# Kernel tuning notes

Measured on AMD Instinct MI355X. Metric: run time of the kernel, lower is better.

## Reference

```python
import math
import jax, jax.numpy as jnp
import numpy as np

B, N, L, D, H = 1, 64, 512, 768, 12
DK = D // H


def setup_inputs() -> dict:
    rng = jax.random.key(0)
    ks = jax.random.split(rng, 8)
    s = 0.02  # weight init scale
    return {
        "query": jax.random.normal(ks[0], (B, N, L, D), jnp.float32),
        "key": jax.random.normal(ks[1], (B, N, L, D), jnp.float32),
        "value": jax.random.normal(ks[2], (B, N, L, D), jnp.float32),
        "Wq": jax.random.normal(ks[3], (D, D), jnp.float32) * s,
        "bq": jnp.zeros((D,), jnp.float32),
        "Wk": jax.random.normal(ks[4], (D, D), jnp.float32) * s,
        "bk": jnp.zeros((D,), jnp.float32),
        "Wv": jax.random.normal(ks[5], (D, D), jnp.float32) * s,
        "bv": jnp.zeros((D,), jnp.float32),
        "Wo": jax.random.normal(ks[6], (D, D), jnp.float32) * s,
        "bo": jnp.zeros((D,), jnp.float32),
    }


def reference(query, key, value, Wq, bq, Wk, bk, Wv, bv, Wo, bo):
    b, n, l, d = query.shape
    h, dk = H, DK
    # combined scaling: 1/sqrt(d_k) * 1/sqrt(N)
    scale = 1.0 / (math.sqrt(dk) * math.sqrt(n))
    # nn.Linear: y = x @ W.T + b  (W is [out, in])
    q = (jnp.einsum('bnld,ed->bnle', query, Wq) + bq).reshape(b, n, l, h, dk) * scale
    k = (jnp.einsum('bnld,ed->bnle', key, Wk) + bk).reshape(b, n, l, h, dk)
    v = (jnp.einsum('bnld,ed->bnle', value, Wv) + bv).reshape(b, n, l, h, dk)
    # tied attention: scores summed over the N (sequence-copy) axis BEFORE softmax
    att = jnp.einsum('bnihk,bnjhk->bhij', q, k)  # [B,H,L,L]
    att = jax.nn.softmax(att, axis=-1)  # dropout is identity in eval
    # single attention map broadcast across all N value tensors
    out = jnp.einsum('bhij,bnjhk->bnihk', att, v).reshape(b, n, l, d)
    return jnp.einsum('bnld,ed->bnle', out, Wo) + bo
```

## Files before the change

kernel.cpp:

```cpp
#include <hip/hip_runtime.h>


typedef __bf16 bf16x8 __attribute__((ext_vector_type(8)));
typedef float f32x4 __attribute__((ext_vector_type(4)));

__device__ __forceinline__ unsigned short f2bf(float f) {
  unsigned u = __float_as_uint(f);
  u += 0x7fffu + ((u >> 16) & 1u);
  return (unsigned short)(u >> 16);
}

__device__ __forceinline__ void gll16(const unsigned short* g, unsigned short* l) {
  __builtin_amdgcn_global_load_lds(
      (const __attribute__((address_space(1))) unsigned int*)g,
      (__attribute__((address_space(3))) unsigned int*)l, 16, 0, 0);
}

#define VMCNT_4 asm volatile("s_waitcnt vmcnt(4)" ::: "memory")
#define VMCNT_0 asm volatile("s_waitcnt vmcnt(0)" ::: "memory")
#define BAR __builtin_amdgcn_s_barrier()

enum { MODE_QCAT = 0, MODE_VT = 1, MODE_ATT = 2, MODE_OUTWS = 3, MODE_OUT_BIAS = 4 };

constexpr int BM = 128, BN = 128, BK = 32;

template <int MODE, bool SWZ, int KS>
__global__ __launch_bounds__(256, 2) void gemm_bt(
    const void* __restrict__ Av, const void* __restrict__ Bv,
    const float* __restrict__ bias, void* __restrict__ Cv,
    int K, int lda, int ldb, long long a_bs, long long b_bs,
    float alpha, int ntn,
    const float* __restrict__ bias2, float alpha2, long long c_bs) {
  constexpr int LP = 32;

  __shared__ unsigned short As0[BM * LP];
  __shared__ unsigned short Bs0[BN * LP];
  __shared__ unsigned short As1[BM * LP];
  __shared__ unsigned short Bs1[BN * LP];

  const int tid = threadIdx.x;
  const int wave = tid >> 6;
  const int lane = tid & 63;
  const int wm = wave >> 1, wn = wave & 1;

  int tm, tn, batch = 0, ks = 0;
  if constexpr (SWZ && MODE == MODE_ATT) {
    const int bid = blockIdx.x;
    const int xcd = bid & 7, j = bid >> 3;
    const int z = (j >> 4) * 8 + xcd;
    const int tile = j & 15;
    tn = tile & 3;
    tm = tile >> 2;
    ks = z % KS;
    batch = z / KS;
  } else if constexpr (SWZ && MODE == MODE_OUTWS) {
    const int bid = blockIdx.x;
    const int xcd = bid & 7, j = bid >> 3;
    const int g = (j >> 6) * 8 + xcd;
    const int idx = j & 63;
    batch = g >> 1;
    tm = idx >> 4;
    tn = (g & 1) * 16 + (idx & 15);
  } else {
    if constexpr (SWZ) {
      const int bid = blockIdx.x;
      const int xcd = bid & 7;
      const int k = bid >> 3;
      tn = k % ntn;
      tm = (k / ntn) * 8 + xcd;
    } else {
      tn = blockIdx.x;
      tm = blockIdx.y;
    }
    batch = blockIdx.z;
    if constexpr (KS > 1) { ks = batch % KS; batch /= KS; }
  }

  const long long m0 = (long long)tm * BM;
  const long long n0 = (long long)tn * BN;

  const unsigned short* Ab = (const unsigned short*)Av + (long long)batch * a_bs + (long long)ks * K;
  const unsigned short* Bb = (const unsigned short*)Bv + (long long)batch * b_bs + (long long)ks * K;

  f32x4 acc[4][4] = {};

  const int l15 = lane & 15;
  const int kq = (lane >> 4) * 8;
  const int r_in = lane >> 2;
  const int c8 = (lane & 3) * 8;

  auto stage = [&](unsigned short* Asb, unsigned short* Bsb, int k0) {
#pragma unroll
    for (int t = 0; t < 2; ++t) {
      const int rb = t * 64 + wave * 16;
      gll16(Ab + (m0 + rb + r_in) * (long long)lda + k0 + c8, &Asb[rb * LP]);
      gll16(Bb + (n0 + rb + r_in) * (long long)ldb + k0 + c8, &Bsb[rb * LP]);
    }
  };
  auto compute = [&](const unsigned short* Asb, const unsigned short* Bsb) {
    bf16x8 af[4], bfr[4];
#pragma unroll
    for (int t = 0; t < 4; ++t)
      af[t] = *(const bf16x8*)&Asb[(wm * 64 + t * 16 + l15) * LP + kq];
#pragma unroll
    for (int u = 0; u < 4; ++u)
      bfr[u] = *(const bf16x8*)&Bsb[(wn * 64 + u * 16 + l15) * LP + kq];
#pragma unroll
    for (int t = 0; t < 4; ++t)
#pragma unroll
      for (int u = 0; u < 4; ++u)
        acc[t][u] = __builtin_amdgcn_mfma_f32_16x16x32_bf16(af[t], bfr[u], acc[t][u], 0, 0, 0);
  };

  float bpre[4] = {};
  float aa = alpha;
  if constexpr (MODE == MODE_QCAT) {
    const float* bb = batch ? bias2 : bias;
    aa = batch ? alpha2 : alpha;
#pragma unroll
    for (int u = 0; u < 4; ++u) bpre[u] = bb[n0 + wn * 64 + u * 16 + l15];
  } else if constexpr (MODE == MODE_VT || MODE == MODE_OUT_BIAS) {
#pragma unroll
    for (int u = 0; u < 4; ++u) bpre[u] = bias[n0 + wn * 64 + u * 16 + l15];
  }

  stage(As0, Bs0, 0);
  VMCNT_0;
  BAR;

  const int NT = K >> 5;
  for (int t = 0; t < NT; t += 2) {
    stage(As1, Bs1, (t + 1) << 5);
    VMCNT_4;
    BAR;
    compute(As0, Bs0);
    BAR;
    if (t + 2 < NT) {
      stage(As0, Bs0, (t + 2) << 5);
      VMCNT_4;
    } else {
      VMCNT_0;
    }
    BAR;
    compute(As1, Bs1);
    BAR;
  }

#pragma unroll
  for (int t = 0; t < 4; ++t) {
#pragma unroll
    for (int u = 0; u < 4; ++u) {
      const long long col = n0 + wn * 64 + u * 16 + l15;
#pragma unroll
      for (int r = 0; r < 4; ++r) {
        const long long row = m0 + wm * 64 + t * 16 + (lane >> 4) * 4 + r;
        float v = acc[t][u][r];
        if constexpr (MODE == MODE_QCAT) {
          v = (v + bpre[u]) * aa;
          const long long h = col >> 6, kk = col & 63, n = row >> 9, i = row & 511;
          ((unsigned short*)Cv + batch * c_bs)[((h * 512 + i) << 12) + (n << 6) + kk] = f2bf(v);
        } else if constexpr (MODE == MODE_VT) {
          v = v + bpre[u];
          const long long h = col >> 6, kk = col & 63, n = row >> 9, j = row & 511;
          ((unsigned short*)Cv)[(((h << 12) + (n << 6) + kk) << 9) + j] = f2bf(v);
        } else if constexpr (MODE == MODE_ATT) {
          float* p = &((float*)Cv)[((long long)batch << 18) + (row << 9) + col];
          if constexpr (KS > 1) atomicAdd(p, v); else *p = v;
        } else if constexpr (MODE == MODE_OUTWS) {
          const long long n = col >> 6, kk = col & 63;
          ((unsigned short*)Cv)[(n * 512 + row) * 768 + (long long)batch * 64 + kk] = f2bf(v);
        } else {
          ((float*)Cv)[row * 768 + col] = v + bpre[u];
        }
      }
    }
  }
}

__global__ __launch_bounds__(256) void softmax_rows(const float* __restrict__ att,
                                                    unsigned short* __restrict__ outb) {
  const long long rowbase = (long long)blockIdx.x << 9;
  const int tid = threadIdx.x;
  float a = att[rowbase + tid];
  float b = att[rowbase + tid + 256];

  float m = fmaxf(a, b);
#pragma unroll
  for (int off = 32; off; off >>= 1) m = fmaxf(m, __shfl_down(m, off));
  __shared__ float redm[4];
  if ((tid & 63) == 0) redm[tid >> 6] = m;
  __syncthreads();
  m = fmaxf(fmaxf(redm[0], redm[1]), fmaxf(redm[2], redm[3]));

  const float e0 = __expf(a - m), e1 = __expf(b - m);
  float s = e0 + e1;
#pragma unroll
  for (int off = 32; off; off >>= 1) s += __shfl_down(s, off);
  __shared__ float reds[4];
  if ((tid & 63) == 0) reds[tid >> 6] = s;
  __syncthreads();
  s = reds[0] + reds[1] + reds[2] + reds[3];

  const float inv = 1.0f / s;
  outb[rowbase + tid] = f2bf(e0 * inv);
  outb[rowbase + tid + 256] = f2bf(e1 * inv);
}

__global__ __launch_bounds__(256) void cvt_bf16(const float* __restrict__ in,
                                                unsigned short* __restrict__ out) {
  const long long i = ((long long)blockIdx.x * 256 + threadIdx.x) * 8;
  const float4 a = *(const float4*)(in + i);
  const float4 b = *(const float4*)(in + i + 4);
  uint4 p;
  p.x = (unsigned)f2bf(a.x) | ((unsigned)f2bf(a.y) << 16);
  p.y = (unsigned)f2bf(a.z) | ((unsigned)f2bf(a.w) << 16);
  p.z = (unsigned)f2bf(b.x) | ((unsigned)f2bf(b.y) << 16);
  p.w = (unsigned)f2bf(b.z) | ((unsigned)f2bf(b.w) << 16);
  *(uint4*)(out + i) = p;
}

__global__ __launch_bounds__(256) void cvt_qk(
    const float* __restrict__ s0, const float* __restrict__ s1,
    unsigned short* __restrict__ d0, unsigned short* __restrict__ d1) {
  const float* s = blockIdx.y ? s1 : s0;
  unsigned short* d = blockIdx.y ? d1 : d0;
  const long long i = ((long long)blockIdx.x * 256 + threadIdx.x) * 8;
  const float4 a = *(const float4*)(s + i);
  const float4 b = *(const float4*)(s + i + 4);
  uint4 p;
  p.x = (unsigned)f2bf(a.x) | ((unsigned)f2bf(a.y) << 16);
  p.y = (unsigned)f2bf(a.z) | ((unsigned)f2bf(a.w) << 16);
  p.z = (unsigned)f2bf(b.x) | ((unsigned)f2bf(b.y) << 16);
  p.w = (unsigned)f2bf(b.z) | ((unsigned)f2bf(b.w) << 16);
  *(uint4*)(d + i) = p;
}

__global__ __launch_bounds__(256) void cvt_w4(
    const float* __restrict__ s0, const float* __restrict__ s1,
    const float* __restrict__ s2, const float* __restrict__ s3,
    unsigned short* __restrict__ d0, unsigned short* __restrict__ d1,
    unsigned short* __restrict__ d2, unsigned short* __restrict__ d3) {
  const float* s;
  unsigned short* d;
  switch (blockIdx.y) {
    case 0: s = s0; d = d0; break;
    case 1: s = s1; d = d1; break;
    case 2: s = s2; d = d2; break;
    default: s = s3; d = d3; break;
  }
  const long long i = ((long long)blockIdx.x * 256 + threadIdx.x) * 8;
  const float4 a = *(const float4*)(s + i);
  const float4 b = *(const float4*)(s + i + 4);
  uint4 p;
  p.x = (unsigned)f2bf(a.x) | ((unsigned)f2bf(a.y) << 16);
  p.y = (unsigned)f2bf(a.z) | ((unsigned)f2bf(a.w) << 16);
  p.z = (unsigned)f2bf(b.x) | ((unsigned)f2bf(b.y) << 16);
  p.w = (unsigned)f2bf(b.z) | ((unsigned)f2bf(b.w) << 16);
  *(uint4*)(d + i) = p;
}

extern "C" void kernel_launch(void* const* d_in, const int* in_sizes, int n_in,
                              void* d_out, int out_size, void* d_ws, size_t ws_size,
                              hipStream_t stream) {
  const float* query = (const float*)d_in[0];
  const float* key   = (const float*)d_in[1];
  const float* value = (const float*)d_in[2];
  const float* Wq = (const float*)d_in[3];
  const float* bq = (const float*)d_in[4];
  const float* Wk = (const float*)d_in[5];
  const float* bk = (const float*)d_in[6];
  const float* Wv = (const float*)d_in[7];
  const float* bv = (const float*)d_in[8];
  const float* Wo = (const float*)d_in[9];
  const float* bo = (const float*)d_in[10];
  float* out = (float*)d_out;

  char* ws = (char*)d_ws;
  unsigned short* q_ws  = (unsigned short*)(ws);
  unsigned short* k_ws  = (unsigned short*)(ws + 50331648);
  unsigned short* vt_ws = (unsigned short*)(ws + 100663296);
  float*          att   = (float*)(ws + 150994944);
  unsigned short* wo_b  = (unsigned short*)(ws + 163577856);
  unsigned short* wq_b  = (unsigned short*)(ws + 150994944);
  unsigned short* wk_b  = (unsigned short*)(ws + 150994944 + 1179648);
  unsigned short* wv_b  = (unsigned short*)(ws + 150994944 + 2359296);
  unsigned short* att_b = k_ws;
  unsigned short* out_ws = q_ws;
  unsigned short* xb0 = (unsigned short*)d_out;
  unsigned short* xb1 = (unsigned short*)d_out + 25165824;

  const dim3 blk(256);

  cvt_w4<<<dim3(288, 4), blk, 0, stream>>>(Wo, Wq, Wk, Wv, wo_b, wq_b, wk_b, wv_b);

  cvt_qk<<<dim3(12288, 2), blk, 0, stream>>>(query, key, xb0, xb1);

  gemm_bt<MODE_QCAT, true, 1><<<dim3(1536, 1, 2), blk, 0, stream>>>(
      xb0, wq_b, bq, q_ws, 768, 768, 768, 25165824LL, 589824LL, 0.015625f, 6,
      bk, 1.0f, 25165824LL);

  cvt_bf16<<<12288, blk, 0, stream>>>(value, xb0);
  gemm_bt<MODE_VT, true, 1><<<dim3(1536, 1, 1), blk, 0, stream>>>(
      xb0, wv_b, bv, vt_ws, 768, 768, 768, 0, 0, 1.0f, 6, nullptr, 0.0f, 0);

  hipMemsetAsync(att, 0, 12582912, stream);
  gemm_bt<MODE_ATT, true, 4><<<dim3(768, 1, 1), blk, 0, stream>>>(
      q_ws, k_ws, nullptr, att, 1024, 4096, 4096, 2097152LL, 2097152LL, 1.0f, 0,
      nullptr, 0.0f, 0);

  softmax_rows<<<6144, blk, 0, stream>>>(att, att_b);

  gemm_bt<MODE_OUTWS, true, 1><<<dim3(1536, 1, 1), blk, 0, stream>>>(
      att_b, vt_ws, nullptr, out_ws, 512, 512, 512, 262144LL, 2097152LL, 1.0f, 0,
      nullptr, 0.0f, 0);

  gemm_bt<MODE_OUT_BIAS, true, 1><<<dim3(1536, 1, 1), blk, 0, stream>>>(
      out_ws, wo_b, bo, out, 768, 768, 768, 0, 0, 1.0f, 6, nullptr, 0.0f, 0);
}
```

Before: 643.3 us.

## Fuse fp32-to-bf16 input conversion into a single batched QKV projection GEMM

```diff
diff --git a/kernel.cpp b/kernel.cpp
--- a/kernel.cpp
+++ b/kernel.cpp
@@ -10,33 +10,29 @@
   return (unsigned short)(u >> 16);
 }
 
-__device__ __forceinline__ void gll16(const unsigned short* g, unsigned short* l) {
+__device__ __forceinline__ void gll16(const void* g, void* l) {
   __builtin_amdgcn_global_load_lds(
       (const __attribute__((address_space(1))) unsigned int*)g,
       (__attribute__((address_space(3))) unsigned int*)l, 16, 0, 0);
 }
 
-#define VMCNT_4 asm volatile("s_waitcnt vmcnt(4)" ::: "memory")
-#define VMCNT_0 asm volatile("s_waitcnt vmcnt(0)" ::: "memory")
 #define BAR __builtin_amdgcn_s_barrier()
 
-enum { MODE_QCAT = 0, MODE_VT = 1, MODE_ATT = 2, MODE_OUTWS = 3, MODE_OUT_BIAS = 4 };
+enum { MODE_PROJ = 0, MODE_ATT = 2, MODE_OUTWS = 3, MODE_OUT_BIAS = 4 };
 
 constexpr int BM = 128, BN = 128, BK = 32;
 
-template <int MODE, bool SWZ, int KS>
+template <int MODE, bool F32A, bool SWZ, int KS>
 __global__ __launch_bounds__(256, 2) void gemm_bt(
-    const void* __restrict__ Av, const void* __restrict__ Bv,
-    const float* __restrict__ bias, void* __restrict__ Cv,
+    const void* __restrict__ A0, const void* __restrict__ A1,
+    const void* __restrict__ A2, const void* __restrict__ Bv,
+    const float* __restrict__ b0, const float* __restrict__ b1,
+    const float* __restrict__ b2, void* __restrict__ Cv,
     int K, int lda, int ldb, long long a_bs, long long b_bs,
-    float alpha, int ntn,
-    const float* __restrict__ bias2, float alpha2, long long c_bs) {
-  constexpr int LP = 32;
-
-  __shared__ unsigned short As0[BM * LP];
-  __shared__ unsigned short Bs0[BN * LP];
-  __shared__ unsigned short As1[BM * LP];
-  __shared__ unsigned short Bs1[BN * LP];
+    float alpha, int ntn, long long c_bs) {
+  __shared__ unsigned short Bs[2][BN * 32];
+  __shared__ float Af32[F32A ? 2 * BM * 32 : 2];
+  __shared__ unsigned short As16[F32A ? 2 : 2 * BM * 32];
 
   const int tid = threadIdx.x;
   const int wave = tid >> 6;
@@ -79,32 +75,83 @@
   const long long m0 = (long long)tm * BM;
   const long long n0 = (long long)tn * BN;
 
-  const unsigned short* Ab = (const unsigned short*)Av + (long long)batch * a_bs + (long long)ks * K;
-  const unsigned short* Bb = (const unsigned short*)Bv + (long long)batch * b_bs + (long long)ks * K;
+  const void* Abase;
+  if constexpr (MODE == MODE_PROJ)
+    Abase = batch == 0 ? A0 : (batch == 1 ? A1 : A2);
+  else
+    Abase = A0;
+  const float* Abf = (const float*)Abase + (long long)batch * a_bs + (long long)ks * K;
+  const unsigned short* Ab16 =
+      (const unsigned short*)Abase + (long long)batch * a_bs + (long long)ks * K;
+  const unsigned short* Bb =
+      (const unsigned short*)Bv + (long long)batch * b_bs + (long long)ks * K;
 
   f32x4 acc[4][4] = {};
 
   const int l15 = lane & 15;
   const int kq = (lane >> 4) * 8;
-  const int r_in = lane >> 2;
-  const int c8 = (lane & 3) * 8;
-
-  auto stage = [&](unsigned short* Asb, unsigned short* Bsb, int k0) {
-#pragma unroll
-    for (int t = 0; t < 2; ++t) {
-      const int rb = t * 64 + wave * 16;
-      gll16(Ab + (m0 + rb + r_in) * (long long)lda + k0 + c8, &Asb[rb * LP]);
-      gll16(Bb + (n0 + rb + r_in) * (long long)ldb + k0 + c8, &Bsb[rb * LP]);
+
+  auto stage = [&](int buf, int k0) {
+    if constexpr (F32A) {
+      const int ra = lane >> 3;
+      const int ca = ((lane & 7) ^ (lane >> 3)) * 4;
+#pragma unroll
+      for (int t = 0; t < 4; ++t) {
+        const int rb = wave * 32 + t * 8;
+        gll16(Abf + (m0 + rb + ra) * (long long)lda + k0 + ca,
+              &Af32[buf * 4096 + rb * 32]);
+      }
+      const int rB = lane >> 2, cB = (lane & 3) * 8;
+#pragma unroll
+      for (int t = 0; t < 2; ++t) {
+        const int rb = wave * 32 + t * 16;
+        gll16(Bb + (n0 + rb + rB) * (long long)ldb + k0 + cB, &Bs[buf][rb * 32]);
+      }
+    } else {
+      const int r_in = lane >> 2, c8 = (lane & 3) * 8;
+#pragma unroll
+      for (int t = 0; t < 2; ++t) {
+        const int rb = t * 64 + wave * 16;
+        gll16(Ab16 + (m0 + rb + r_in) * (long long)lda + k0 + c8,
+              &As16[buf * 4096 + rb * 32]);
+        gll16(Bb + (n0 + rb + r_in) * (long long)ldb + k0 + c8, &Bs[buf][rb * 32]);
+      }
     }
   };
-  auto compute = [&](const unsigned short* Asb, const unsigned short* Bsb) {
+
+  auto wait_cur = [&]() {
+    if constexpr (F32A)
+      asm volatile("s_waitcnt vmcnt(6)" ::: "memory");
+    else
+      asm volatile("s_waitcnt vmcnt(4)" ::: "memory");
+  };
+
+  auto compute = [&](int buf) {
     bf16x8 af[4], bfr[4];
-#pragma unroll
-    for (int t = 0; t < 4; ++t)
-      af[t] = *(const bf16x8*)&Asb[(wm * 64 + t * 16 + l15) * LP + kq];
+    if constexpr (F32A) {
+#pragma unroll
+      for (int t = 0; t < 4; ++t) {
+        const int row = wm * 64 + t * 16 + l15;
+        const int sw = row & 7;
+        const int c0 = kq >> 2;
+        const float* base = &Af32[buf * 4096 + row * 32];
+        f32x4 lo = *(const f32x4*)(base + ((c0 ^ sw) << 2));
+        f32x4 hi = *(const f32x4*)(base + (((c0 + 1) ^ sw) << 2));
+        bf16x8 a;
+        a[0] = (__bf16)lo[0]; a[1] = (__bf16)lo[1];
+        a[2] = (__bf16)lo[2]; a[3] = (__bf16)lo[3];
+        a[4] = (__bf16)hi[0]; a[5] = (__bf16)hi[1];
+        a[6] = (__bf16)hi[2]; a[7] = (__bf16)hi[3];
+        af[t] = a;
+      }
+    } else {
+#pragma unroll
+      for (int t = 0; t < 4; ++t)
+        af[t] = *(const bf16x8*)&As16[buf * 4096 + (wm * 64 + t * 16 + l15) * 32 + kq];
+    }
 #pragma unroll
     for (int u = 0; u < 4; ++u)
-      bfr[u] = *(const bf16x8*)&Bsb[(wn * 64 + u * 16 + l15) * LP + kq];
+      bfr[u] = *(const bf16x8*)&Bs[buf][(wn * 64 + u * 16 + l15) * 32 + kq];
 #pragma unroll
     for (int t = 0; t < 4; ++t)
 #pragma unroll
@@ -114,35 +161,35 @@
 
   float bpre[4] = {};
   float aa = alpha;
-  if constexpr (MODE == MODE_QCAT) {
-    const float* bb = batch ? bias2 : bias;
-    aa = batch ? alpha2 : alpha;
+  if constexpr (MODE == MODE_PROJ) {
+    const float* bb = batch == 0 ? b0 : (batch == 1 ? b1 : b2);
+    aa = batch == 0 ? alpha : 1.0f;
 #pragma unroll
     for (int u = 0; u < 4; ++u) bpre[u] = bb[n0 + wn * 64 + u * 16 + l15];
-  } else if constexpr (MODE == MODE_VT || MODE == MODE_OUT_BIAS) {
-#pragma unroll
-    for (int u = 0; u < 4; ++u) bpre[u] = bias[n0 + wn * 64 + u * 16 + l15];
-  }
-
-  stage(As0, Bs0, 0);
-  VMCNT_0;
+  } else if constexpr (MODE == MODE_OUT_BIAS) {
+#pragma unroll
+    for (int u = 0; u < 4; ++u) bpre[u] = b0[n0 + wn * 64 + u * 16 + l15];
+  }
+
+  stage(0, 0);
+  asm volatile("s_waitcnt vmcnt(0)" ::: "memory");
   BAR;
 
   const int NT = K >> 5;
   for (int t = 0; t < NT; t += 2) {
-    stage(As1, Bs1, (t + 1) << 5);
-    VMCNT_4;
+    stage(1, (t + 1) << 5);
+    wait_cur();
     BAR;
-    compute(As0, Bs0);
+    compute(0);
     BAR;
     if (t + 2 < NT) {
-      stage(As0, Bs0, (t + 2) << 5);
-      VMCNT_4;
+      stage(0, (t + 2) << 5);
+      wait_cur();
     } else {
-      VMCNT_0;
+      asm volatile("s_waitcnt vmcnt(0)" ::: "memory");
     }
     BAR;
-    compute(As1, Bs1);
+    compute(1);
     BAR;
   }
 
@@ -155,14 +202,18 @@
       for (int r = 0; r < 4; ++r) {
         const long long row = m0 + wm * 64 + t * 16 + (lane >> 4) * 4 + r;
         float v = acc[t][u][r];
-        if constexpr (MODE == MODE_QCAT) {
-          v = (v + bpre[u]) * aa;
-          const long long h = col >> 6, kk = col & 63, n = row >> 9, i = row & 511;
-          ((unsigned short*)Cv + batch * c_bs)[((h * 512 + i) << 12) + (n << 6) + kk] = f2bf(v);
-        } else if constexpr (MODE == MODE_VT) {
-          v = v + bpre[u];
-          const long long h = col >> 6, kk = col & 63, n = row >> 9, j = row & 511;
-          ((unsigned short*)Cv)[(((h << 12) + (n << 6) + kk) << 9) + j] = f2bf(v);
+        if constexpr (MODE == MODE_PROJ) {
+          if (batch < 2) {
+            const float vv = (v + bpre[u]) * aa;
+            const long long h = col >> 6, kk = col & 63, n = row >> 9, i = row & 511;
+            ((unsigned short*)Cv + batch * c_bs)[((h * 512 + i) << 12) + (n << 6) + kk] =
+                f2bf(vv);
+          } else {
+            const float vv = v + bpre[u];
+            const long long h = col >> 6, kk = col & 63, n = row >> 9, j = row & 511;
+            ((unsigned short*)Cv + 2 * c_bs)[(((h << 12) + (n << 6) + kk) << 9) + j] =
+                f2bf(vv);
+          }
         } else if constexpr (MODE == MODE_ATT) {
           float* p = &((float*)Cv)[((long long)batch << 18) + (row << 9) + col];
           if constexpr (KS > 1) atomicAdd(p, v); else *p = v;
@@ -204,35 +255,6 @@
   const float inv = 1.0f / s;
   outb[rowbase + tid] = f2bf(e0 * inv);
   outb[rowbase + tid + 256] = f2bf(e1 * inv);
-}
-
-__global__ __launch_bounds__(256) void cvt_bf16(const float* __restrict__ in,
-                                                unsigned short* __restrict__ out) {
-  const long long i = ((long long)blockIdx.x * 256 + threadIdx.x) * 8;
-  const float4 a = *(const float4*)(in + i);
-  const float4 b = *(const float4*)(in + i + 4);
-  uint4 p;
-  p.x = (unsigned)f2bf(a.x) | ((unsigned)f2bf(a.y) << 16);
-  p.y = (unsigned)f2bf(a.z) | ((unsigned)f2bf(a.w) << 16);
-  p.z = (unsigned)f2bf(b.x) | ((unsigned)f2bf(b.y) << 16);
-  p.w = (unsigned)f2bf(b.z) | ((unsigned)f2bf(b.w) << 16);
-  *(uint4*)(out + i) = p;
-}
-
-__global__ __launch_bounds__(256) void cvt_qk(
-    const float* __restrict__ s0, const float* __restrict__ s1,
-    unsigned short* __restrict__ d0, unsigned short* __restrict__ d1) {
-  const float* s = blockIdx.y ? s1 : s0;
-  unsigned short* d = blockIdx.y ? d1 : d0;
-  const long long i = ((long long)blockIdx.x * 256 + threadIdx.x) * 8;
-  const float4 a = *(const float4*)(s + i);
-  const float4 b = *(const float4*)(s + i + 4);
-  uint4 p;
-  p.x = (unsigned)f2bf(a.x) | ((unsigned)f2bf(a.y) << 16);
-  p.y = (unsigned)f2bf(a.z) | ((unsigned)f2bf(a.w) << 16);
-  p.z = (unsigned)f2bf(b.x) | ((unsigned)f2bf(b.y) << 16);
-  p.w = (unsigned)f2bf(b.z) | ((unsigned)f2bf(b.w) << 16);
-  *(uint4*)(d + i) = p;
 }
 
 __global__ __launch_bounds__(256) void cvt_w4(
@@ -286,34 +308,28 @@
   unsigned short* wv_b  = (unsigned short*)(ws + 150994944 + 2359296);
   unsigned short* att_b = k_ws;
   unsigned short* out_ws = q_ws;
-  unsigned short* xb0 = (unsigned short*)d_out;
-  unsigned short* xb1 = (unsigned short*)d_out + 25165824;
+  (void)wk_b; (void)wv_b; (void)vt_ws;
 
   const dim3 blk(256);
 
   cvt_w4<<<dim3(288, 4), blk, 0, stream>>>(Wo, Wq, Wk, Wv, wo_b, wq_b, wk_b, wv_b);
 
-  cvt_qk<<<dim3(12288, 2), blk, 0, stream>>>(query, key, xb0, xb1);
-
-  gemm_bt<MODE_QCAT, true, 1><<<dim3(1536, 1, 2), blk, 0, stream>>>(
-      xb0, wq_b, bq, q_ws, 768, 768, 768, 25165824LL, 589824LL, 0.015625f, 6,
-      bk, 1.0f, 25165824LL);
-
-  cvt_bf16<<<12288, blk, 0, stream>>>(value, xb0);
-  gemm_bt<MODE_VT, true, 1><<<dim3(1536, 1, 1), blk, 0, stream>>>(
-      xb0, wv_b, bv, vt_ws, 768, 768, 768, 0, 0, 1.0f, 6, nullptr, 0.0f, 0);
+  gemm_bt<MODE_PROJ, true, true, 1><<<dim3(1536, 1, 3), blk, 0, stream>>>(
+      query, key, value, wq_b, bq, bk, bv, q_ws,
+      768, 768, 768, 0, 589824LL, 0.015625f, 6, 25165824LL);
 
   hipMemsetAsync(att, 0, 12582912, stream);
-  gemm_bt<MODE_ATT, true, 4><<<dim3(768, 1, 1), blk, 0, stream>>>(
-      q_ws, k_ws, nullptr, att, 1024, 4096, 4096, 2097152LL, 2097152LL, 1.0f, 0,
-      nullptr, 0.0f, 0);
+  gemm_bt<MODE_ATT, false, true, 4><<<dim3(768, 1, 1), blk, 0, stream>>>(
+      q_ws, nullptr, nullptr, k_ws, nullptr, nullptr, nullptr, att,
+      1024, 4096, 4096, 2097152LL, 2097152LL, 1.0f, 0, 0);
 
   softmax_rows<<<6144, blk, 0, stream>>>(att, att_b);
 
-  gemm_bt<MODE_OUTWS, true, 1><<<dim3(1536, 1, 1), blk, 0, stream>>>(
-      att_b, vt_ws, nullptr, out_ws, 512, 512, 512, 262144LL, 2097152LL, 1.0f, 0,
-      nullptr, 0.0f, 0);
-
-  gemm_bt<MODE_OUT_BIAS, true, 1><<<dim3(1536, 1, 1), blk, 0, stream>>>(
-      out_ws, wo_b, bo, out, 768, 768, 768, 0, 0, 1.0f, 6, nullptr, 0.0f, 0);
-}
+  gemm_bt<MODE_OUTWS, false, true, 1><<<dim3(1536, 1, 1), blk, 0, stream>>>(
+      att_b, nullptr, nullptr, vt_ws, nullptr, nullptr, nullptr, out_ws,
+      512, 512, 512, 262144LL, 2097152LL, 1.0f, 0, 0);
+
+  gemm_bt<MODE_OUT_BIAS, false, true, 1><<<dim3(1536, 1, 1), blk, 0, stream>>>(
+      out_ws, nullptr, nullptr, wo_b, bo, nullptr, nullptr, out,
+      768, 768, 768, 0, 0, 1.0f, 6, 0);
+}
```

New measurement: 687.9 us. 1.07x slower.

## Add 256x256-tile 512-thread GEMM for the projection GEMMs with swizzled LDS pipeline

Applied to the files above, without the earlier changes.

```diff
diff --git a/kernel.cpp b/kernel.cpp
--- a/kernel.cpp
+++ b/kernel.cpp
@@ -10,17 +10,151 @@
   return (unsigned short)(u >> 16);
 }
 
-__device__ __forceinline__ void gll16(const unsigned short* g, unsigned short* l) {
+__device__ __forceinline__ void gll16(const void* g, void* l) {
   __builtin_amdgcn_global_load_lds(
       (const __attribute__((address_space(1))) unsigned int*)g,
       (__attribute__((address_space(3))) unsigned int*)l, 16, 0, 0);
 }
 
-#define VMCNT_4 asm volatile("s_waitcnt vmcnt(4)" ::: "memory")
-#define VMCNT_0 asm volatile("s_waitcnt vmcnt(0)" ::: "memory")
 #define BAR __builtin_amdgcn_s_barrier()
 
 enum { MODE_QCAT = 0, MODE_VT = 1, MODE_ATT = 2, MODE_OUTWS = 3, MODE_OUT_BIAS = 4 };
+
+template <int MODE>
+__global__ __launch_bounds__(512, 2) void gemm256(
+    const void* __restrict__ Av, const void* __restrict__ Bv,
+    const float* __restrict__ b0, const float* __restrict__ b1,
+    void* __restrict__ Cv, int K, int lda, int ldb,
+    long long a_bs, long long b_bs, float alpha0, float alpha1,
+    long long c_bs, int ntn) {
+  __shared__ unsigned short L[2][2][16384];
+
+  const int tid = threadIdx.x;
+  const int wave = tid >> 6;
+  const int lane = tid & 63;
+  const int wm = wave >> 2;
+  const int wn = wave & 3;
+  const int l15 = lane & 15;
+  const int kq8 = lane >> 4;
+  const int sw = l15 & 7;
+
+  const int bid = blockIdx.x;
+  const int xcd = bid & 7;
+  const int kk_ = bid >> 3;
+  const int tn = kk_ % ntn;
+  const int tm = (kk_ / ntn) * 8 + xcd;
+  const int batch = blockIdx.z;
+
+  const long long m0 = (long long)tm * 256;
+  const long long n0 = (long long)tn * 256;
+
+  const unsigned short* Ab = (const unsigned short*)Av + (long long)batch * a_bs;
+  const unsigned short* Bb = (const unsigned short*)Bv + (long long)batch * b_bs;
+
+  const long long rowAw = m0 + wave * 8 + (lane >> 3);
+  const long long rowBw = n0 + wave * 8 + (lane >> 3);
+  const int csw = ((lane & 7) ^ (lane >> 3)) << 3;
+
+  f32x4 acc[8][4] = {};
+
+  auto stA = [&](int buf, int q, int k0) {
+    gll16(Ab + (rowAw + (q << 6)) * (long long)lda + k0 + csw,
+          &L[buf][0][(q << 12) + (wave << 9)]);
+  };
+  auto stB = [&](int buf, int q, int k0) {
+    gll16(Bb + (rowBw + (q << 6)) * (long long)ldb + k0 + csw,
+          &L[buf][1][(q << 12) + (wave << 9)]);
+  };
+
+  float bpre[4] = {};
+  float aa = 1.0f;
+  if constexpr (MODE == MODE_QCAT || MODE == MODE_VT || MODE == MODE_OUT_BIAS) {
+    const float* bb = batch ? b1 : b0;
+    aa = batch ? alpha1 : alpha0;
+#pragma unroll
+    for (int u = 0; u < 4; ++u) bpre[u] = bb[n0 + wn * 64 + u * 16 + l15];
+  }
+
+  const int NT = K >> 6;
+#pragma unroll
+  for (int q = 0; q < 4; ++q) stB(0, q, 0);
+#pragma unroll
+  for (int q = 0; q < 4; ++q) stA(0, q, 0);
+  if (NT > 1) {
+    stA(1, 0, 64);
+    stA(1, 2, 64);
+    asm volatile("s_waitcnt vmcnt(2)" ::: "memory");
+  } else {
+    asm volatile("s_waitcnt vmcnt(0)" ::: "memory");
+  }
+  BAR;
+
+  for (int T = 0; T < NT; ++T) {
+    const int cur = T & 1, nxt = cur ^ 1;
+    const int k1 = (T + 1) << 6, k2 = (T + 2) << 6;
+#pragma unroll
+    for (int p = 0; p < 4; ++p) {
+      const int kc = p >> 1, mh = p & 1;
+      bf16x8 af[4], bfr[4];
+#pragma unroll
+      for (int mf = 0; mf < 4; ++mf) {
+        const int row = wm * 128 + mh * 64 + mf * 16 + l15;
+        af[mf] = *(const bf16x8*)&L[cur][0][row * 64 + (((kc << 2) + kq8) ^ sw) * 8];
+      }
+#pragma unroll
+      for (int u = 0; u < 4; ++u) {
+        const int row = wn * 64 + u * 16 + l15;
+        bfr[u] = *(const bf16x8*)&L[cur][1][row * 64 + (((kc << 2) + kq8) ^ sw) * 8];
+      }
+      if (p == 0 && T + 1 < NT) { stB(nxt, 0, k1); stB(nxt, 1, k1); }
+      if (p == 1 && T + 1 < NT) { stB(nxt, 2, k1); stB(nxt, 3, k1); }
+      if (p == 2 && T + 1 < NT) { stA(nxt, 1, k1); stA(nxt, 3, k1); }
+      if (p == 3 && T + 2 < NT) { stA(cur, 0, k2); stA(cur, 2, k2); }
+      __builtin_amdgcn_s_setprio(1);
+#pragma unroll
+      for (int mf = 0; mf < 4; ++mf)
+#pragma unroll
+        for (int u = 0; u < 4; ++u)
+          acc[mh * 4 + mf][u] = __builtin_amdgcn_mfma_f32_16x16x32_bf16(
+              af[mf], bfr[u], acc[mh * 4 + mf][u], 0, 0, 0);
+      __builtin_amdgcn_s_setprio(0);
+      if (p == 3) {
+        if (T + 1 < NT) {
+          if (T + 2 < NT) asm volatile("s_waitcnt vmcnt(2)" ::: "memory");
+          else            asm volatile("s_waitcnt vmcnt(0)" ::: "memory");
+          BAR;
+        }
+      } else {
+        BAR;
+      }
+    }
+  }
+
+#pragma unroll
+  for (int mf = 0; mf < 8; ++mf) {
+#pragma unroll
+    for (int u = 0; u < 4; ++u) {
+      const long long col = n0 + wn * 64 + u * 16 + l15;
+#pragma unroll
+      for (int r = 0; r < 4; ++r) {
+        const long long row = m0 + wm * 128 + mf * 16 + (lane >> 4) * 4 + r;
+        float v = acc[mf][u][r];
+        if constexpr (MODE == MODE_QCAT) {
+          const float vv = (v + bpre[u]) * aa;
+          const long long h = col >> 6, kq = col & 63, n = row >> 9, i = row & 511;
+          ((unsigned short*)Cv + batch * c_bs)[((h * 512 + i) << 12) + (n << 6) + kq] =
+              f2bf(vv);
+        } else if constexpr (MODE == MODE_VT) {
+          const float vv = v + bpre[u];
+          const long long h = col >> 6, kq = col & 63, n = row >> 9, j = row & 511;
+          ((unsigned short*)Cv)[(((h << 12) + (n << 6) + kq) << 9) + j] = f2bf(vv);
+        } else {
+          ((float*)Cv)[row * 768 + col] = v + bpre[u];
+        }
+      }
+    }
+  }
+}
 
 constexpr int BM = 128, BN = 128, BK = 32;
 
@@ -29,8 +163,7 @@
     const void* __restrict__ Av, const void* __restrict__ Bv,
     const float* __restrict__ bias, void* __restrict__ Cv,
     int K, int lda, int ldb, long long a_bs, long long b_bs,
-    float alpha, int ntn,
-    const float* __restrict__ bias2, float alpha2, long long c_bs) {
+    float alpha, int ntn, long long c_bs) {
   constexpr int LP = 32;
 
   __shared__ unsigned short As0[BM * LP];
@@ -112,34 +245,22 @@
         acc[t][u] = __builtin_amdgcn_mfma_f32_16x16x32_bf16(af[t], bfr[u], acc[t][u], 0, 0, 0);
   };
 
-  float bpre[4] = {};
-  float aa = alpha;
-  if constexpr (MODE == MODE_QCAT) {
-    const float* bb = batch ? bias2 : bias;
-    aa = batch ? alpha2 : alpha;
-#pragma unroll
-    for (int u = 0; u < 4; ++u) bpre[u] = bb[n0 + wn * 64 + u * 16 + l15];
-  } else if constexpr (MODE == MODE_VT || MODE == MODE_OUT_BIAS) {
-#pragma unroll
-    for (int u = 0; u < 4; ++u) bpre[u] = bias[n0 + wn * 64 + u * 16 + l15];
-  }
-
   stage(As0, Bs0, 0);
-  VMCNT_0;
+  asm volatile("s_waitcnt vmcnt(0)" ::: "memory");
   BAR;
 
   const int NT = K >> 5;
   for (int t = 0; t < NT; t += 2) {
     stage(As1, Bs1, (t + 1) << 5);
-    VMCNT_4;
+    asm volatile("s_waitcnt vmcnt(4)" ::: "memory");
     BAR;
     compute(As0, Bs0);
     BAR;
     if (t + 2 < NT) {
       stage(As0, Bs0, (t + 2) << 5);
-      VMCNT_4;
+      asm volatile("s_waitcnt vmcnt(4)" ::: "memory");
     } else {
-      VMCNT_0;
+      asm volatile("s_waitcnt vmcnt(0)" ::: "memory");
     }
     BAR;
     compute(As1, Bs1);
@@ -155,22 +276,14 @@
       for (int r = 0; r < 4; ++r) {
         const long long row = m0 + wm * 64 + t * 16 + (lane >> 4) * 4 + r;
         float v = acc[t][u][r];
-        if constexpr (MODE == MODE_QCAT) {
-          v = (v + bpre[u]) * aa;
-          const long long h = col >> 6, kk = col & 63, n = row >> 9, i = row & 511;
-          ((unsigned short*)Cv + batch * c_bs)[((h * 512 + i) << 12) + (n << 6) + kk] = f2bf(v);
-        } else if constexpr (MODE == MODE_VT) {
-          v = v + bpre[u];
-          const long long h = col >> 6, kk = col & 63, n = row >> 9, j = row & 511;
-          ((unsigned short*)Cv)[(((h << 12) + (n << 6) + kk) << 9) + j] = f2bf(v);
-        } else if constexpr (MODE == MODE_ATT) {
+        if constexpr (MODE == MODE_ATT) {
           float* p = &((float*)Cv)[((long long)batch << 18) + (row << 9) + col];
           if constexpr (KS > 1) atomicAdd(p, v); else *p = v;
         } else if constexpr (MODE == MODE_OUTWS) {
           const long long n = col >> 6, kk = col & 63;
           ((unsigned short*)Cv)[(n * 512 + row) * 768 + (long long)batch * 64 + kk] = f2bf(v);
         } else {
-          ((float*)Cv)[row * 768 + col] = v + bpre[u];
+          ((float*)Cv)[row * 768 + col] = v + alpha;
         }
       }
     }
@@ -288,32 +401,32 @@
   unsigned short* out_ws = q_ws;
   unsigned short* xb0 = (unsigned short*)d_out;
   unsigned short* xb1 = (unsigned short*)d_out + 25165824;
+  (void)wk_b; (void)wv_b;
 
   const dim3 blk(256);
+  const dim3 blk5(512);
 
   cvt_w4<<<dim3(288, 4), blk, 0, stream>>>(Wo, Wq, Wk, Wv, wo_b, wq_b, wk_b, wv_b);
 
   cvt_qk<<<dim3(12288, 2), blk, 0, stream>>>(query, key, xb0, xb1);
 
-  gemm_bt<MODE_QCAT, true, 1><<<dim3(1536, 1, 2), blk, 0, stream>>>(
-      xb0, wq_b, bq, q_ws, 768, 768, 768, 25165824LL, 589824LL, 0.015625f, 6,
-      bk, 1.0f, 25165824LL);
+  gemm256<MODE_QCAT><<<dim3(384, 1, 2), blk5, 0, stream>>>(
+      xb0, wq_b, bq, bk, q_ws, 768, 768, 768, 25165824LL, 589824LL,
+      0.015625f, 1.0f, 25165824LL, 3);
 
   cvt_bf16<<<12288, blk, 0, stream>>>(value, xb0);
-  gemm_bt<MODE_VT, true, 1><<<dim3(1536, 1, 1), blk, 0, stream>>>(
-      xb0, wv_b, bv, vt_ws, 768, 768, 768, 0, 0, 1.0f, 6, nullptr, 0.0f, 0);
+  gemm256<MODE_VT><<<dim3(384, 1, 1), blk5, 0, stream>>>(
+      xb0, wv_b, bv, nullptr, vt_ws, 768, 768, 768, 0, 0, 1.0f, 1.0f, 0, 3);
 
   hipMemsetAsync(att, 0, 12582912, stream);
   gemm_bt<MODE_ATT, true, 4><<<dim3(768, 1, 1), blk, 0, stream>>>(
-      q_ws, k_ws, nullptr, att, 1024, 4096, 4096, 2097152LL, 2097152LL, 1.0f, 0,
-      nullptr, 0.0f, 0);
+      q_ws, k_ws, nullptr, att, 1024, 4096, 4096, 2097152LL, 2097152LL, 1.0f, 0, 0);
 
   softmax_rows<<<6144, blk, 0, stream>>>(att, att_b);
 
   gemm_bt<MODE_OUTWS, true, 1><<<dim3(1536, 1, 1), blk, 0, stream>>>(
-      att_b, vt_ws, nullptr, out_ws, 512, 512, 512, 262144LL, 2097152LL, 1.0f, 0,
-      nullptr, 0.0f, 0);
-
-  gemm_bt<MODE_OUT_BIAS, true, 1><<<dim3(1536, 1, 1), blk, 0, stream>>>(
-      out_ws, wo_b, bo, out, 768, 768, 768, 0, 0, 1.0f, 6, nullptr, 0.0f, 0);
-}
+      att_b, vt_ws, nullptr, out_ws, 512, 512, 512, 262144LL, 2097152LL, 1.0f, 0, 0);
+
+  gemm256<MODE_OUT_BIAS><<<dim3(384, 1, 1), blk5, 0, stream>>>(
+      out_ws, wo_b, bo, nullptr, out, 768, 768, 768, 0, 0, 1.0f, 1.0f, 0, 3);
+}
```

After: 633.3 us. No clear change (-1.6%).
